# Optimization experiments

Measured on AMD Instinct MI355X. Metric: run time of the kernel, lower is better.

The kernel has to match this reference:

```python
import jax, jax.numpy as jnp
import numpy as np

NUM_NODES = 1_000_000
IN_FEATS = 128
N_HIDDEN = 256
N_CLASSES = 47
# block sizes: fanouts [15,10,5], batch 1024
N_SRC = [1081344, 67584, 6144]
N_DST = [67584, 6144, 1024]
N_EDGE = [1013760, 61440, 5120]


def setup_inputs() -> dict:
    key = jax.random.key(0)
    ks = jax.random.split(key, 16)
    inp = {}
    inp["emb_table"] = jax.random.normal(ks[0], (NUM_NODES, IN_FEATS), dtype=jnp.float32)
    inp["input_nodes"] = jax.random.randint(ks[1], (N_SRC[0],), 0, NUM_NODES)
    for l in range(3):
        inp[f"src{l}"] = jax.random.randint(ks[2 + 2 * l], (N_EDGE[l],), 0, N_SRC[l])
        inp[f"dst{l}"] = jax.random.randint(ks[3 + 2 * l], (N_EDGE[l],), 0, N_DST[l])
    dims = [(IN_FEATS, N_HIDDEN), (N_HIDDEN, N_HIDDEN), (N_HIDDEN, N_CLASSES)]
    for l, (din, dout) in enumerate(dims):
        s = 1.0 / np.sqrt(din)
        inp[f"Wself{l}"] = jax.random.uniform(ks[8 + 2 * l], (din, dout), minval=-s, maxval=s, dtype=jnp.float32)
        inp[f"Wneigh{l}"] = jax.random.uniform(ks[9 + 2 * l], (din, dout), minval=-s, maxval=s, dtype=jnp.float32)
        inp[f"b{l}"] = jnp.zeros((dout,), dtype=jnp.float32)
    return inp


def _sage_layer(h, src, dst, n_dst, Wself, Wneigh, b):
    # DGL SAGEConv 'mean': out = fc_self(h_dst) + fc_neigh(mean_{u in N(v)} h_u) + bias
    h_dst = h[:n_dst]
    msg = h[src]                                   # [E, din] irregular gather
    agg = jax.ops.segment_sum(msg, dst, num_segments=n_dst)
    deg = jax.ops.segment_sum(jnp.ones((src.shape[0],), h.dtype), dst, num_segments=n_dst)
    agg = agg / jnp.maximum(deg, 1.0)[:, None]     # segment mean (0-degree -> 0)
    return h_dst @ Wself + agg @ Wneigh + b


def reference(emb_table, Wself0, Wneigh0, b0, Wself1, Wneigh1, b1, Wself2, Wneigh2, b2,
              input_nodes, src0, dst0, src1, dst1, src2, dst2):
    h = emb_table[input_nodes]                     # embedding lookup
    params = [(src0, dst0, N_DST[0], Wself0, Wneigh0, b0),
              (src1, dst1, N_DST[1], Wself1, Wneigh1, b1),
              (src2, dst2, N_DST[2], Wself2, Wneigh2, b2)]
    for l, (s, d, nd, Ws, Wn, b) in enumerate(params):
        h = _sage_layer(h, s, d, nd, Ws, Wn, b)
        if l != 2:
            h = jax.nn.relu(h)                     # dropout p=0 -> identity
    return h
```

## Files before the change

### kernel.cpp

```cpp
#include <hip/hip_runtime.h>
#include <cstdint>
#include <cstddef>

#define NDST0 67584
#define NDST1 6144
#define NDST2 1024
#define NEDGE0 1013760
#define NEDGE1 61440
#define NEDGE2 5120
#define F0 128
#define F1 256
#define NCLS 47

typedef unsigned short ushort_t;
typedef __attribute__((ext_vector_type(8))) short short8;
typedef __attribute__((ext_vector_type(8))) unsigned short ushortx8;
typedef __attribute__((ext_vector_type(4))) float floatx4;

__device__ __forceinline__ ushort_t f2bf(float f) {
    union { float f; unsigned u; } v; v.f = f;
    unsigned r = v.u + 0x7fffu + ((v.u >> 16) & 1u);
    return (ushort_t)(r >> 16);
}
__device__ __forceinline__ float bf2f(ushort_t u) {
    union { unsigned u; float f; } v; v.u = ((unsigned)u) << 16;
    return v.f;
}

__device__ __forceinline__ void async_copy16(ushort_t* lds, const ushort_t* g) {
    __builtin_amdgcn_global_load_lds(
        (const __attribute__((address_space(1))) unsigned*)(g),
        (__attribute__((address_space(3))) unsigned*)(lds),
        16, 0, 0);
}

#define SEL_BLOCKS  8448
#define WPREP_BLOCKS 1024
#define HIST_BLOCKS 1024

__device__ __forceinline__ void wprep_seg(
    const float* __restrict__ Ws, const float* __restrict__ Wn,
    int din, int dout, int id, ushort_t* __restrict__ Bt)
{
    const int K2 = 2 * din;
    const int n = id / K2;
    const int k2 = id - n * K2;
    float v = 0.f;
    if (n < dout)
        v = (k2 < din) ? Ws[(size_t)k2 * dout + n] : Wn[(size_t)(k2 - din) * dout + n];
    Bt[id] = f2bf(v);
}

__global__ __launch_bounds__(256) void prep_all(
    const float* __restrict__ emb, const int* __restrict__ input_nodes,
    ushort_t* __restrict__ embsel,
    const float* __restrict__ Ws0, const float* __restrict__ Wn0,
    const float* __restrict__ Ws1, const float* __restrict__ Wn1,
    const float* __restrict__ Ws2, const float* __restrict__ Wn2,
    ushort_t* __restrict__ Bt0, ushort_t* __restrict__ Bt1,
    ushort_t* __restrict__ Bt2,
    const int* __restrict__ dst0, const int* __restrict__ dst1,
    const int* __restrict__ dst2,
    int* __restrict__ cnt0, int* __restrict__ cnt1, int* __restrict__ cnt2)
{
    const int b = blockIdx.x;
    const int tid = threadIdx.x;
    if (b < SEL_BLOCKS) {
        const int q = b * 256 + tid;
        const int qpr = F0 >> 2;
        if (q >= NDST0 * qpr) return;
        const int m = q >> 5;
        const int c = q & 31;
        const int row = input_nodes[m];
        const float4 v = *(const float4*)(emb + (size_t)row * F0 + c * 4);
        ushort4 o;
        o.x = f2bf(v.x); o.y = f2bf(v.y); o.z = f2bf(v.z); o.w = f2bf(v.w);
        *(ushort4*)(embsel + (size_t)m * F0 + c * 4) = o;
    } else if (b < SEL_BLOCKS + WPREP_BLOCKS) {
        const int S0 = 256 * 256, S1 = 256 * 512, S2 = 128 * 512;
        const int id = (b - SEL_BLOCKS) * 256 + tid;
        if (id < S0)                 wprep_seg(Ws0, Wn0, F0, 256,  id,           Bt0);
        else if (id < S0 + S1)       wprep_seg(Ws1, Wn1, F1, 256,  id - S0,      Bt1);
        else if (id < S0 + S1 + S2)  wprep_seg(Ws2, Wn2, F1, NCLS, id - S0 - S1, Bt2);
    } else {
        const int total = NEDGE0 + NEDGE1 + NEDGE2;
        int i = (b - SEL_BLOCKS - WPREP_BLOCKS) * 256 + tid;
        const int stride = HIST_BLOCKS * 256;
        for (; i < total; i += stride) {
            if (i < NEDGE0)                 atomicAdd(&cnt0[dst0[i]], 1);
            else if (i < NEDGE0 + NEDGE1)   atomicAdd(&cnt1[dst1[i - NEDGE0]], 1);
            else                            atomicAdd(&cnt2[dst2[i - NEDGE0 - NEDGE1]], 1);
        }
    }
}

__global__ __launch_bounds__(1024) void scan_all(
    const int* __restrict__ c0, int* __restrict__ r0, int* __restrict__ w0,
    const int* __restrict__ c1, int* __restrict__ r1, int* __restrict__ w1,
    const int* __restrict__ c2, int* __restrict__ r2, int* __restrict__ w2)
{
    __shared__ int sums[1024];
    const int* cnt; int* rs; int* work; int n;
    if (blockIdx.x == 0)      { cnt = c0; rs = r0; work = w0; n = NDST0; }
    else if (blockIdx.x == 1) { cnt = c1; rs = r1; work = w1; n = NDST1; }
    else                      { cnt = c2; rs = r2; work = w2; n = NDST2; }

    const int tid = threadIdx.x;
    const int L = (n + 1023) >> 10;
    const int lo = tid * L;
    const int hi = (lo + L < n) ? (lo + L) : n;
    int s = 0;
    for (int i = lo; i < hi; ++i) s += cnt[i];
    sums[tid] = s;
    __syncthreads();
    int v = s;
    for (int off = 1; off < 1024; off <<= 1) {
        int t = (tid >= off) ? sums[tid - off] : 0;
        __syncthreads();
        v += t;
        sums[tid] = v;
        __syncthreads();
    }
    int run = v - s;
    for (int i = lo; i < hi; ++i) {
        rs[i] = run;
        work[i] = run;
        run += cnt[i];
    }
    if (tid == 1023) rs[n] = run;
}

__global__ __launch_bounds__(256) void fill_all(
    const int* __restrict__ src0, const int* __restrict__ dst0,
    const int* __restrict__ src1, const int* __restrict__ dst1,
    const int* __restrict__ src2, const int* __restrict__ dst2,
    const int* __restrict__ idx,
    int* __restrict__ work0, int* __restrict__ work1, int* __restrict__ work2,
    int* __restrict__ esrc0, int* __restrict__ esrc1, int* __restrict__ esrc2)
{
    int e = blockIdx.x * 256 + threadIdx.x;
    if (e < NEDGE0) {
        const int s = src0[e];
        const int row = idx[s];
        const int p = atomicAdd(&work0[dst0[e]], 1);
        esrc0[p] = row;
    } else if (e < NEDGE0 + NEDGE1) {
        e -= NEDGE0;
        const int p = atomicAdd(&work1[dst1[e]], 1);
        esrc1[p] = src1[e];
    } else if (e < NEDGE0 + NEDGE1 + NEDGE2) {
        e -= NEDGE0 + NEDGE1;
        const int p = atomicAdd(&work2[dst2[e]], 1);
        esrc2[p] = src2[e];
    }
}

__global__ __launch_bounds__(256) void gather_f32(
    const float* __restrict__ table, const int* __restrict__ esrc,
    const int* __restrict__ rs, const int* __restrict__ cnt,
    int nd, int feat, int lshift, ushort_t* __restrict__ agg)
{
    const int lanes = 1 << lshift;
    const int gpb = 256 >> lshift;
    const int d = blockIdx.x * gpb + ((int)threadIdx.x >> lshift);
    if (d >= nd) return;
    const int lane = (int)threadIdx.x & (lanes - 1);
    const int start = rs[d];
    const int c = cnt[d];
    const float* tb = table + (size_t)lane * 4;
    float4 acc = make_float4(0.f, 0.f, 0.f, 0.f);
    int i = 0;
    for (; i + 3 < c; i += 4) {
        const int r0 = esrc[start + i];
        const int r1 = esrc[start + i + 1];
        const int r2 = esrc[start + i + 2];
        const int r3 = esrc[start + i + 3];
        const float4 v0 = *(const float4*)(tb + (size_t)r0 * feat);
        const float4 v1 = *(const float4*)(tb + (size_t)r1 * feat);
        const float4 v2 = *(const float4*)(tb + (size_t)r2 * feat);
        const float4 v3 = *(const float4*)(tb + (size_t)r3 * feat);
        acc.x += (v0.x + v1.x) + (v2.x + v3.x);
        acc.y += (v0.y + v1.y) + (v2.y + v3.y);
        acc.z += (v0.z + v1.z) + (v2.z + v3.z);
        acc.w += (v0.w + v1.w) + (v2.w + v3.w);
    }
    for (; i < c; ++i) {
        const int r0 = esrc[start + i];
        const float4 v0 = *(const float4*)(tb + (size_t)r0 * feat);
        acc.x += v0.x; acc.y += v0.y; acc.z += v0.z; acc.w += v0.w;
    }
    const float sc = 1.0f / fmaxf((float)c, 1.0f);
    ushort4 o;
    o.x = f2bf(acc.x * sc); o.y = f2bf(acc.y * sc);
    o.z = f2bf(acc.z * sc); o.w = f2bf(acc.w * sc);
    *(ushort4*)(agg + (size_t)d * feat + lane * 4) = o;
}

__global__ __launch_bounds__(256) void gather_bf16(
    const ushort_t* __restrict__ table, const int* __restrict__ esrc,
    const int* __restrict__ rs, const int* __restrict__ cnt,
    int nd, int feat, int lshift, ushort_t* __restrict__ agg)
{
    const int lanes = 1 << lshift;
    const int gpb = 256 >> lshift;
    const int d = blockIdx.x * gpb + ((int)threadIdx.x >> lshift);
    if (d >= nd) return;
    const int lane = (int)threadIdx.x & (lanes - 1);
    const int start = rs[d];
    const int c = cnt[d];
    const ushort_t* tb = table + (size_t)lane * 8;
    float acc[8] = {0.f, 0.f, 0.f, 0.f, 0.f, 0.f, 0.f, 0.f};
    int i = 0;
    for (; i + 1 < c; i += 2) {
        const int r0 = esrc[start + i];
        const int r1 = esrc[start + i + 1];
        const ushortx8 v0 = *(const ushortx8*)(tb + (size_t)r0 * feat);
        const ushortx8 v1 = *(const ushortx8*)(tb + (size_t)r1 * feat);
        #pragma unroll
        for (int j = 0; j < 8; ++j) acc[j] += bf2f(v0[j]) + bf2f(v1[j]);
    }
    if (i < c) {
        const int r0 = esrc[start + i];
        const ushortx8 v0 = *(const ushortx8*)(tb + (size_t)r0 * feat);
        #pragma unroll
        for (int j = 0; j < 8; ++j) acc[j] += bf2f(v0[j]);
    }
    const float sc = 1.0f / fmaxf((float)c, 1.0f);
    ushortx8 o;
    #pragma unroll
    for (int j = 0; j < 8; ++j) o[j] = f2bf(acc[j] * sc);
    *(ushortx8*)(agg + (size_t)d * feat + lane * 8) = o;
}

__global__ __launch_bounds__(256) void mfma_gemm(
    const ushort_t* __restrict__ Aself, const ushort_t* __restrict__ Aneigh,
    const ushort_t* __restrict__ Bt, const float* __restrict__ bias,
    void* __restrict__ outp, int din, int dout, int out_bf16, int do_relu)
{
    __shared__ ushort_t As[128 * 32];
    __shared__ ushort_t Bs[128 * 32];

    const int tid  = threadIdx.x;
    const int wave = tid >> 6;
    const int lane = tid & 63;
    const int m0 = blockIdx.x * 128;
    const int n0 = blockIdx.y * 128;
    const int wm = (wave & 1) * 64;
    const int wn = (wave >> 1) * 64;

    const int arow = lane >> 2;
    const int achk = (lane & 3) * 8;

    const int K2 = 2 * din;

    floatx4 acc[4][4];
    const floatx4 zero = {0.f, 0.f, 0.f, 0.f};
    #pragma unroll
    for (int i = 0; i < 4; ++i)
        #pragma unroll
        for (int j = 0; j < 4; ++j) acc[i][j] = zero;

    const int fr = lane & 15;
    const int fq = (lane >> 4) * 8;

    for (int k0 = 0; k0 < K2; k0 += 32) {
        const ushort_t* Abase = (k0 < din) ? (Aself + k0) : (Aneigh + (k0 - din));
        #pragma unroll
        for (int i = 0; i < 2; ++i) {
            const int rg = (wave * 2 + i) * 16 + arow;
            async_copy16(&As[rg * 32 + achk],
                         Abase + (size_t)(m0 + rg) * din + achk);
            async_copy16(&Bs[rg * 32 + achk],
                         Bt + (size_t)(n0 + rg) * K2 + k0 + achk);
        }
        __syncthreads();

        short8 a[4], b[4];
        #pragma unroll
        for (int f = 0; f < 4; ++f) {
            a[f] = *(const short8*)&As[(wm + f * 16 + fr) * 32 + fq];
            b[f] = *(const short8*)&Bs[(wn + f * 16 + fr) * 32 + fq];
        }
        #pragma unroll
        for (int fm = 0; fm < 4; ++fm)
            #pragma unroll
            for (int fn = 0; fn < 4; ++fn)
                acc[fm][fn] = __builtin_amdgcn_mfma_f32_16x16x32_bf16(
                    a[fm], b[fn], acc[fm][fn], 0, 0, 0);
        __syncthreads();
    }

    const int erow = (lane >> 4) * 4;
    const int ecol = lane & 15;
    #pragma unroll
    for (int fn = 0; fn < 4; ++fn) {
        const int gn = n0 + wn + fn * 16 + ecol;
        if (gn >= dout) continue;
        const float bv = bias[gn];
        #pragma unroll
        for (int fm = 0; fm < 4; ++fm) {
            #pragma unroll
            for (int r = 0; r < 4; ++r) {
                const size_t gm = m0 + wm + fm * 16 + erow + r;
                float v = acc[fm][fn][r] + bv;
                if (do_relu) v = fmaxf(v, 0.f);
                if (out_bf16) ((ushort_t*)outp)[gm * dout + gn] = f2bf(v);
                else          ((float*)outp)[gm * dout + gn] = v;
            }
        }
    }
}

extern "C" void kernel_launch(void* const* d_in, const int* in_sizes, int n_in,
                              void* d_out, int out_size, void* d_ws, size_t ws_size,
                              hipStream_t stream)
{
    const float* emb         = (const float*)d_in[0];
    const int*   input_nodes = (const int*)d_in[1];
    const int*   src0 = (const int*)d_in[2];
    const int*   dst0 = (const int*)d_in[3];
    const int*   src1 = (const int*)d_in[4];
    const int*   dst1 = (const int*)d_in[5];
    const int*   src2 = (const int*)d_in[6];
    const int*   dst2 = (const int*)d_in[7];
    const float* Ws0 = (const float*)d_in[8];
    const float* Wn0 = (const float*)d_in[9];
    const float* b0  = (const float*)d_in[10];
    const float* Ws1 = (const float*)d_in[11];
    const float* Wn1 = (const float*)d_in[12];
    const float* b1  = (const float*)d_in[13];
    const float* Ws2 = (const float*)d_in[14];
    const float* Wn2 = (const float*)d_in[15];
    const float* b2  = (const float*)d_in[16];
    float* out = (float*)d_out;

    ushort_t* us     = (ushort_t*)d_ws;
    ushort_t* embsel = us;
    ushort_t* agg0   = embsel + (size_t)NDST0 * F0;
    ushort_t* h1     = agg0 + (size_t)NDST0 * F0;
    ushort_t* agg1   = h1 + (size_t)NDST0 * F1;
    ushort_t* h2     = agg1 + (size_t)NDST1 * F1;
    ushort_t* agg2   = h2 + (size_t)NDST1 * F1;
    ushort_t* Bt0    = agg2 + (size_t)NDST2 * F1;
    ushort_t* Bt1    = Bt0 + 256 * 256;
    ushort_t* Bt2    = Bt1 + 256 * 512;

    int* ip   = (int*)(Bt2 + 128 * 512);
    int* cnt0 = ip;  ip += NDST0;
    int* cnt1 = ip;  ip += NDST1;
    int* cnt2 = ip;  ip += NDST2;
    const size_t zero_bytes = (size_t)(NDST0 + NDST1 + NDST2) * sizeof(int);
    int* rs0   = ip; ip += NDST0 + 1;
    int* work0 = ip; ip += NDST0;
    int* rs1   = ip; ip += NDST1 + 1;
    int* work1 = ip; ip += NDST1;
    int* rs2   = ip; ip += NDST2 + 1;
    int* work2 = ip; ip += NDST2;
    int* esrc0 = ip; ip += NEDGE0;
    int* esrc1 = ip; ip += NEDGE1;
    int* esrc2 = ip; ip += NEDGE2;

    hipMemsetAsync(cnt0, 0, zero_bytes, stream);

    prep_all<<<SEL_BLOCKS + WPREP_BLOCKS + HIST_BLOCKS, 256, 0, stream>>>(
        emb, input_nodes, embsel,
        Ws0, Wn0, Ws1, Wn1, Ws2, Wn2, Bt0, Bt1, Bt2,
        dst0, dst1, dst2, cnt0, cnt1, cnt2);

    scan_all<<<3, 1024, 0, stream>>>(cnt0, rs0, work0, cnt1, rs1, work1, cnt2, rs2, work2);
    fill_all<<<(NEDGE0 + NEDGE1 + NEDGE2 + 255) / 256, 256, 0, stream>>>(
        src0, dst0, src1, dst1, src2, dst2, input_nodes,
        work0, work1, work2, esrc0, esrc1, esrc2);

    gather_f32<<<NDST0 / 8, 256, 0, stream>>>(emb, esrc0, rs0, cnt0, NDST0, F0, 5, agg0);
    mfma_gemm<<<dim3(NDST0 / 128, 256 / 128), 256, 0, stream>>>(
        embsel, agg0, Bt0, b0, h1, F0, 256, 1, 1);

    gather_bf16<<<NDST1 / 8, 256, 0, stream>>>(h1, esrc1, rs1, cnt1, NDST1, F1, 5, agg1);
    mfma_gemm<<<dim3(NDST1 / 128, 256 / 128), 256, 0, stream>>>(
        h1, agg1, Bt1, b1, h2, F1, 256, 1, 1);

    gather_bf16<<<NDST2 / 8, 256, 0, stream>>>(h2, esrc2, rs2, cnt2, NDST2, F1, 5, agg2);
    mfma_gemm<<<dim3(NDST2 / 128, 1), 256, 0, stream>>>(
        h2, agg2, Bt2, b2, out, F1, NCLS, 0, 0);
}
```

Before: 988.6 us.

## Record per-edge ranks in histogram pass to remove second atomic pass in CSR fill

The histogram pass now stores the value returned by atomicAdd as a per-edge rank. The fill kernel then computes each edge's slot as row_start[dst] + rank without any atomics, and the separate work-counter copy is dropped from the scan. This costs an extra write and read of about one million ints per layer-0 edge set. Separately, the GEMM grid is swapped so the N-tile index varies fastest, which makes the two N tiles of the same M rows run as adjacent blocks and share the A tile in cache.

Measured after the change: 923.5 us. 1.07x faster.

```diff
diff --git a/kernel.cpp b/kernel.cpp
--- a/kernel.cpp
+++ b/kernel.cpp
@@ -61,7 +61,8 @@
     ushort_t* __restrict__ Bt2,
     const int* __restrict__ dst0, const int* __restrict__ dst1,
     const int* __restrict__ dst2,
-    int* __restrict__ cnt0, int* __restrict__ cnt1, int* __restrict__ cnt2)
+    int* __restrict__ cnt0, int* __restrict__ cnt1, int* __restrict__ cnt2,
+    int* __restrict__ rank0, int* __restrict__ rank1, int* __restrict__ rank2)
 {
     const int b = blockIdx.x;
     const int tid = threadIdx.x;
@@ -87,23 +88,29 @@
         int i = (b - SEL_BLOCKS - WPREP_BLOCKS) * 256 + tid;
         const int stride = HIST_BLOCKS * 256;
         for (; i < total; i += stride) {
-            if (i < NEDGE0)                 atomicAdd(&cnt0[dst0[i]], 1);
-            else if (i < NEDGE0 + NEDGE1)   atomicAdd(&cnt1[dst1[i - NEDGE0]], 1);
-            else                            atomicAdd(&cnt2[dst2[i - NEDGE0 - NEDGE1]], 1);
+            if (i < NEDGE0) {
+                rank0[i] = atomicAdd(&cnt0[dst0[i]], 1);
+            } else if (i < NEDGE0 + NEDGE1) {
+                const int j = i - NEDGE0;
+                rank1[j] = atomicAdd(&cnt1[dst1[j]], 1);
+            } else {
+                const int j = i - NEDGE0 - NEDGE1;
+                rank2[j] = atomicAdd(&cnt2[dst2[j]], 1);
+            }
         }
     }
 }
 
 __global__ __launch_bounds__(1024) void scan_all(
-    const int* __restrict__ c0, int* __restrict__ r0, int* __restrict__ w0,
-    const int* __restrict__ c1, int* __restrict__ r1, int* __restrict__ w1,
-    const int* __restrict__ c2, int* __restrict__ r2, int* __restrict__ w2)
+    const int* __restrict__ c0, int* __restrict__ r0,
+    const int* __restrict__ c1, int* __restrict__ r1,
+    const int* __restrict__ c2, int* __restrict__ r2)
 {
     __shared__ int sums[1024];
-    const int* cnt; int* rs; int* work; int n;
-    if (blockIdx.x == 0)      { cnt = c0; rs = r0; work = w0; n = NDST0; }
-    else if (blockIdx.x == 1) { cnt = c1; rs = r1; work = w1; n = NDST1; }
-    else                      { cnt = c2; rs = r2; work = w2; n = NDST2; }
+    const int* cnt; int* rs; int n;
+    if (blockIdx.x == 0)      { cnt = c0; rs = r0; n = NDST0; }
+    else if (blockIdx.x == 1) { cnt = c1; rs = r1; n = NDST1; }
+    else                      { cnt = c2; rs = r2; n = NDST2; }
 
     const int tid = threadIdx.x;
     const int L = (n + 1023) >> 10;
@@ -124,7 +131,6 @@
     int run = v - s;
     for (int i = lo; i < hi; ++i) {
         rs[i] = run;
-        work[i] = run;
         run += cnt[i];
     }
     if (tid == 1023) rs[n] = run;
@@ -135,23 +141,22 @@
     const int* __restrict__ src1, const int* __restrict__ dst1,
     const int* __restrict__ src2, const int* __restrict__ dst2,
     const int* __restrict__ idx,
-    int* __restrict__ work0, int* __restrict__ work1, int* __restrict__ work2,
+    const int* __restrict__ rs0, const int* __restrict__ rs1,
+    const int* __restrict__ rs2,
+    const int* __restrict__ rank0, const int* __restrict__ rank1,
+    const int* __restrict__ rank2,
     int* __restrict__ esrc0, int* __restrict__ esrc1, int* __restrict__ esrc2)
 {
     int e = blockIdx.x * 256 + threadIdx.x;
     if (e < NEDGE0) {
-        const int s = src0[e];
-        const int row = idx[s];
-        const int p = atomicAdd(&work0[dst0[e]], 1);
-        esrc0[p] = row;
+        const int row = idx[src0[e]];
+        esrc0[rs0[dst0[e]] + rank0[e]] = row;
     } else if (e < NEDGE0 + NEDGE1) {
         e -= NEDGE0;
-        const int p = atomicAdd(&work1[dst1[e]], 1);
-        esrc1[p] = src1[e];
+        esrc1[rs1[dst1[e]] + rank1[e]] = src1[e];
     } else if (e < NEDGE0 + NEDGE1 + NEDGE2) {
         e -= NEDGE0 + NEDGE1;
-        const int p = atomicAdd(&work2[dst2[e]], 1);
-        esrc2[p] = src2[e];
+        esrc2[rs2[dst2[e]] + rank2[e]] = src2[e];
     }
 }
 
@@ -243,8 +248,8 @@
     const int tid  = threadIdx.x;
     const int wave = tid >> 6;
     const int lane = tid & 63;
-    const int m0 = blockIdx.x * 128;
-    const int n0 = blockIdx.y * 128;
+    const int m0 = blockIdx.y * 128;
+    const int n0 = blockIdx.x * 128;
     const int wm = (wave & 1) * 64;
     const int wn = (wave >> 1) * 64;
 
@@ -351,11 +356,11 @@
     int* cnt2 = ip;  ip += NDST2;
     const size_t zero_bytes = (size_t)(NDST0 + NDST1 + NDST2) * sizeof(int);
     int* rs0   = ip; ip += NDST0 + 1;
-    int* work0 = ip; ip += NDST0;
     int* rs1   = ip; ip += NDST1 + 1;
-    int* work1 = ip; ip += NDST1;
     int* rs2   = ip; ip += NDST2 + 1;
-    int* work2 = ip; ip += NDST2;
+    int* rank0 = ip; ip += NEDGE0;
+    int* rank1 = ip; ip += NEDGE1;
+    int* rank2 = ip; ip += NEDGE2;
     int* esrc0 = ip; ip += NEDGE0;
     int* esrc1 = ip; ip += NEDGE1;
     int* esrc2 = ip; ip += NEDGE2;
@@ -365,22 +370,22 @@
     prep_all<<<SEL_BLOCKS + WPREP_BLOCKS + HIST_BLOCKS, 256, 0, stream>>>(
         emb, input_nodes, embsel,
         Ws0, Wn0, Ws1, Wn1, Ws2, Wn2, Bt0, Bt1, Bt2,
-        dst0, dst1, dst2, cnt0, cnt1, cnt2);
-
-    scan_all<<<3, 1024, 0, stream>>>(cnt0, rs0, work0, cnt1, rs1, work1, cnt2, rs2, work2);
+        dst0, dst1, dst2, cnt0, cnt1, cnt2, rank0, rank1, rank2);
+
+    scan_all<<<3, 1024, 0, stream>>>(cnt0, rs0, cnt1, rs1, cnt2, rs2);
     fill_all<<<(NEDGE0 + NEDGE1 + NEDGE2 + 255) / 256, 256, 0, stream>>>(
         src0, dst0, src1, dst1, src2, dst2, input_nodes,
-        work0, work1, work2, esrc0, esrc1, esrc2);
+        rs0, rs1, rs2, rank0, rank1, rank2, esrc0, esrc1, esrc2);
 
     gather_f32<<<NDST0 / 8, 256, 0, stream>>>(emb, esrc0, rs0, cnt0, NDST0, F0, 5, agg0);
-    mfma_gemm<<<dim3(NDST0 / 128, 256 / 128), 256, 0, stream>>>(
+    mfma_gemm<<<dim3(256 / 128, NDST0 / 128), 256, 0, stream>>>(
         embsel, agg0, Bt0, b0, h1, F0, 256, 1, 1);
 
     gather_bf16<<<NDST1 / 8, 256, 0, stream>>>(h1, esrc1, rs1, cnt1, NDST1, F1, 5, agg1);
-    mfma_gemm<<<dim3(NDST1 / 128, 256 / 128), 256, 0, stream>>>(
+    mfma_gemm<<<dim3(256 / 128, NDST1 / 128), 256, 0, stream>>>(
         h1, agg1, Bt1, b1, h2, F1, 256, 1, 1);
 
     gather_bf16<<<NDST2 / 8, 256, 0, stream>>>(h2, esrc2, rs2, cnt2, NDST2, F1, 5, agg2);
-    mfma_gemm<<<dim3(NDST2 / 128, 1), 256, 0, stream>>>(
+    mfma_gemm<<<dim3(1, NDST2 / 128), 256, 0, stream>>>(
         h2, agg2, Bt2, b2, out, F1, NCLS, 0, 0);
 }
```
